# Kernel optimization log

Measured on AMD Instinct MI355X. Metric: run time of the kernel, lower is better.

Reference implementation:

```python
import jax, jax.numpy as jnp
import numpy as np

N_EMBD = 128
N_HEAD = 4
HEAD_DIM = N_EMBD // N_HEAD  # 32


def setup_inputs() -> dict:
    key = jax.random.key(0)
    k_x, k_wqkv, k_bqkv, k_wp, k_bp = jax.random.split(key, 5)
    B, T = 8, 2048
    x = jax.random.normal(k_x, (B, T, N_EMBD), dtype=jnp.float32)
    # torch Linear(n_embd, 3*n_embd): weight [out,in]; store as [in,out] for x @ W
    scale = 1.0 / np.sqrt(N_EMBD)
    w_qkv = jax.random.uniform(k_wqkv, (N_EMBD, 3 * N_EMBD), minval=-scale, maxval=scale, dtype=jnp.float32)
    b_qkv = jax.random.uniform(k_bqkv, (3 * N_EMBD,), minval=-scale, maxval=scale, dtype=jnp.float32)
    w_proj = jax.random.uniform(k_wp, (N_EMBD, N_EMBD), minval=-scale, maxval=scale, dtype=jnp.float32)
    b_proj = jax.random.uniform(k_bp, (N_EMBD,), minval=-scale, maxval=scale, dtype=jnp.float32)
    return {"x": x, "w_qkv": w_qkv, "b_qkv": b_qkv, "w_proj": w_proj, "b_proj": b_proj}


def reference(x, w_qkv, b_qkv, w_proj, b_proj):
    B, T, C = x.shape
    H, D = N_HEAD, HEAD_DIM
    qkv = x @ w_qkv + b_qkv  # [B,T,3C]
    q, k, v = jnp.split(qkv, 3, axis=2)
    # [B,T,C] -> [B,H,T,D]
    q = q.reshape(B, T, H, D).transpose(0, 2, 1, 3)
    k = k.reshape(B, T, H, D).transpose(0, 2, 1, 3)
    v = v.reshape(B, T, H, D).transpose(0, 2, 1, 3)
    scale = 1.0 / np.sqrt(D).astype(np.float32)
    logits = jnp.einsum("bhqd,bhkd->bhqk", q, k) * scale  # [B,H,T,T]
    causal = jnp.tril(jnp.ones((T, T), dtype=bool))
    logits = jnp.where(causal, logits, jnp.finfo(logits.dtype).min)
    attn = jax.nn.softmax(logits, axis=-1)
    y = jnp.einsum("bhqk,bhkd->bhqd", attn, v)  # [B,H,T,D]
    y = y.transpose(0, 2, 1, 3).reshape(B, T, C)
    y = y @ w_proj + b_proj
    # dropout is identity in eval/inference mode
    return y
```

## Files before the change

### kernel.cpp

```cpp
#include <hip/hip_runtime.h>
#include <hip/hip_bf16.h>
#include <stdint.h>


#define T_SEQ 2048
#define C_EMBD 128
#define NH 4
#define HD 32
#define BATCH 8
#define BHT (BATCH * NH)

typedef float f4  __attribute__((ext_vector_type(4)));
typedef short bh8 __attribute__((ext_vector_type(8)));
typedef unsigned long long ull;

__device__ __forceinline__ unsigned short f2bf(float f) {
    union { float f; unsigned u; } v; v.f = f;
    return (unsigned short)((v.u + 0x7fffu + ((v.u >> 16) & 1u)) >> 16);
}
__device__ __forceinline__ ull pk4(float a, float b, float c, float d) {
    return (ull)f2bf(a) | ((ull)f2bf(b) << 16) | ((ull)f2bf(c) << 32) | ((ull)f2bf(d) << 48);
}

__global__ __launch_bounds__(256) void qkv_mfma(const float* __restrict__ x,
                                                const float* __restrict__ w,
                                                const float* __restrict__ bias,
                                                unsigned short* __restrict__ qb,
                                                unsigned short* __restrict__ kb,
                                                unsigned short* __restrict__ vtb) {
    constexpr int XR = 136;
    constexpr int WR = 136;
    constexpr int VR = 72;
    __shared__ __align__(16) unsigned short xs[64 * XR];
    __shared__ __align__(16) unsigned short wt[128 * WR];
    __shared__ __align__(16) unsigned short vt[128 * VR];

    const int nt = blockIdx.x;
    const int mt = blockIdx.y;
    const int t0g = mt * 64;
    const int b = t0g >> 11;
    const int t0 = t0g & 2047;
    const int tid = threadIdx.x;
    const int wave = tid >> 6;
    const int lane = tid & 63;
    const int col = lane & 15;
    const int quad = lane >> 4;

    for (int i = 0; i < 8; ++i) {
        const int idx = tid + i * 256;
        const int row = idx >> 5, c4 = idx & 31;
        const float4 xv = *(const float4*)(x + (size_t)(t0g + row) * C_EMBD + c4 * 4);
        *(ull*)(&xs[row * XR + c4 * 4]) = pk4(xv.x, xv.y, xv.z, xv.w);
    }
    for (int i = 0; i < 16; ++i) {
        const int idx = tid + i * 256;
        const int n = idx & 127, k4 = idx >> 7;
        const float w0 = w[(k4 * 4 + 0) * 384 + nt * 128 + n];
        const float w1 = w[(k4 * 4 + 1) * 384 + nt * 128 + n];
        const float w2 = w[(k4 * 4 + 2) * 384 + nt * 128 + n];
        const float w3 = w[(k4 * 4 + 3) * 384 + nt * 128 + n];
        *(ull*)(&wt[n * WR + k4 * 4]) = pk4(w0, w1, w2, w3);
    }
    __syncthreads();

    f4 acc[8];
#pragma unroll
    for (int nf = 0; nf < 8; ++nf) {
        const float bv = bias[nt * 128 + nf * 16 + col];
        acc[nf] = (f4){bv, bv, bv, bv};
    }
#pragma unroll
    for (int ch = 0; ch < 4; ++ch) {
        const bh8 af = *(const bh8*)(&xs[(wave * 16 + col) * XR + ch * 32 + quad * 8]);
#pragma unroll
        for (int nf = 0; nf < 8; ++nf) {
            const bh8 bf = *(const bh8*)(&wt[(nf * 16 + col) * WR + ch * 32 + quad * 8]);
            acc[nf] = __builtin_amdgcn_mfma_f32_16x16x32_bf16(af, bf, acc[nf], 0, 0, 0);
        }
    }

    const int mrow = wave * 16 + quad * 4;
    if (nt < 2) {
        unsigned short* outp = (nt == 0) ? qb : kb;
        const float sc = (nt == 0) ? 0.25503485952317864f : 1.0f;
#pragma unroll
        for (int nf = 0; nf < 8; ++nf) {
            const int n = nf * 16 + col, h = n >> 5, d = n & 31;
            const size_t base = ((size_t)(b * NH + h) * T_SEQ + t0 + mrow) * HD + d;
#pragma unroll
            for (int r = 0; r < 4; ++r)
                outp[base + (size_t)r * HD] = f2bf(acc[nf][r] * sc);
        }
    } else {
#pragma unroll
        for (int nf = 0; nf < 8; ++nf) {
            const int n = nf * 16 + col;
#pragma unroll
            for (int r = 0; r < 4; ++r)
                vt[n * VR + mrow + r] = f2bf(acc[nf][r]);
        }
        __syncthreads();
        for (int i = 0; i < 16; ++i) {
            const int idx = tid + i * 256;
            const int c = idx >> 5, dw = idx & 31;
            const int h2 = c >> 5, d2 = c & 31;
            const unsigned v0 = *(const unsigned*)(&vt[c * VR + dw * 2]);
            *(unsigned*)(vtb + ((size_t)(b * NH + h2) * HD + d2) * T_SEQ + t0 + dw * 2) = v0;
        }
    }
}

__global__ __launch_bounds__(256, 4) void attn(const unsigned short* __restrict__ qb,
                                               const unsigned short* __restrict__ kb,
                                               const unsigned short* __restrict__ vtb,
                                               unsigned short* __restrict__ y) {
    constexpr int KROW = 40;
    constexpr int VROW = 72;
    constexpr int PROW = 72;
    __shared__ __align__(16) unsigned short Ks[2][64 * KROW];
    __shared__ __align__(16) unsigned short Vt[2][32 * VROW];
    __shared__ __align__(16) unsigned short Pb[4][16 * PROW];

    const int bid = blockIdx.x;
    const int bh = bid & 31;
    const int pr = bid >> 5;
    const int tid = threadIdx.x;
    const int wave = tid >> 6;
    const int lane = tid & 63;
    const int col = lane & 15;
    const int quad = lane >> 4;

    const unsigned short* kbase = kb + (size_t)bh * T_SEQ * HD;
    const unsigned short* vbase = vtb + (size_t)bh * HD * T_SEQ;
    const int ks_t = tid >> 2, ks_q = tid & 3;
    const int vs_d = tid >> 3, vs_s = tid & 7;

    for (int ph = 0; ph < 2; ++ph) {
        const int qt = ph ? pr : (31 - pr);
        const int q0 = qt * 64;
        const int ntiles = qt + 1;

        const bh8 qfrag = *(const bh8*)(qb + ((size_t)bh * T_SEQ + q0 + wave * 16 + col) * HD + quad * 8);
        f4 yacc0 = {0.f, 0.f, 0.f, 0.f}, yacc1 = {0.f, 0.f, 0.f, 0.f};
        float rs[4] = {0.f, 0.f, 0.f, 0.f};

        uint4 kreg = *(const uint4*)(kbase + (size_t)ks_t * HD + ks_q * 8);
        uint4 vreg = *(const uint4*)(vbase + (size_t)vs_d * T_SEQ + vs_s * 8);

        for (int kt = 0; kt < ntiles; ++kt) {
            const int buf = kt & 1;
            *(uint4*)(&Ks[buf][ks_t * KROW + ks_q * 8]) = kreg;
            *(uint4*)(&Vt[buf][vs_d * VROW + vs_s * 8]) = vreg;
            if (kt + 1 < ntiles) {
                kreg = *(const uint4*)(kbase + (size_t)((kt + 1) * 64 + ks_t) * HD + ks_q * 8);
                vreg = *(const uint4*)(vbase + (size_t)vs_d * T_SEQ + (kt + 1) * 64 + vs_s * 8);
            }
            __syncthreads();

            const bool diag = (kt == qt);
            f4 z[4];
#pragma unroll
            for (int f = 0; f < 4; ++f) {
                if (diag && f > wave) {
                    z[f] = (f4){-1e30f, -1e30f, -1e30f, -1e30f};
                } else {
                    const bh8 kfrag = *(const bh8*)(&Ks[buf][(f * 16 + col) * KROW + quad * 8]);
                    f4 zz = {0.f, 0.f, 0.f, 0.f};
                    zz = __builtin_amdgcn_mfma_f32_16x16x32_bf16(qfrag, kfrag, zz, 0, 0, 0);
                    if (diag && f == wave) {
#pragma unroll
                        for (int r = 0; r < 4; ++r)
                            if (col > quad * 4 + r) zz[r] = -1e30f;
                    }
                    z[f] = zz;
                }
            }
#pragma unroll
            for (int f = 0; f < 4; ++f)
#pragma unroll
                for (int r = 0; r < 4; ++r) {
                    const float pv = __builtin_amdgcn_exp2f(z[f][r]);
                    rs[r] += pv;
                    Pb[wave][(quad * 4 + r) * PROW + f * 16 + col] = f2bf(pv);
                }
#pragma unroll
            for (int kk = 0; kk < 2; ++kk) {
                const bh8 pf = *(const bh8*)(&Pb[wave][col * PROW + kk * 32 + quad * 8]);
                const bh8 v0 = *(const bh8*)(&Vt[buf][col * VROW + kk * 32 + quad * 8]);
                yacc0 = __builtin_amdgcn_mfma_f32_16x16x32_bf16(pf, v0, yacc0, 0, 0, 0);
                const bh8 v1 = *(const bh8*)(&Vt[buf][(16 + col) * VROW + kk * 32 + quad * 8]);
                yacc1 = __builtin_amdgcn_mfma_f32_16x16x32_bf16(pf, v1, yacc1, 0, 0, 0);
            }
        }

        const int bb = bh >> 2, hh = bh & 3;
        unsigned short* yp = y + ((size_t)bb * T_SEQ + q0 + wave * 16) * C_EMBD + hh * HD;
#pragma unroll
        for (int r = 0; r < 4; ++r) {
            float t = rs[r];
            t += __shfl_xor(t, 1);
            t += __shfl_xor(t, 2);
            t += __shfl_xor(t, 4);
            t += __shfl_xor(t, 8);
            const float inv = 1.0f / t;
            yp[(quad * 4 + r) * C_EMBD + col] = f2bf(yacc0[r] * inv);
            yp[(quad * 4 + r) * C_EMBD + 16 + col] = f2bf(yacc1[r] * inv);
        }
        __syncthreads();
    }
}

__global__ __launch_bounds__(256) void out_mfma(const unsigned short* __restrict__ y,
                                                const float* __restrict__ w,
                                                const float* __restrict__ bias,
                                                float* __restrict__ out) {
    constexpr int YR = 136;
    constexpr int WR = 136;
    __shared__ __align__(16) unsigned short ys[64 * YR];
    __shared__ __align__(16) unsigned short wt[128 * WR];

    const int mt = blockIdx.x;
    const int row0 = mt * 64;
    const int tid = threadIdx.x;
    const int wave = tid >> 6;
    const int lane = tid & 63;
    const int col = lane & 15;
    const int quad = lane >> 4;

    for (int i = 0; i < 4; ++i) {
        const int idx = tid + i * 256;
        const int row = idx >> 4, q8 = idx & 15;
        const uint4 v = *(const uint4*)(y + (size_t)(row0 + row) * C_EMBD + q8 * 8);
        *(uint4*)(&ys[row * YR + q8 * 8]) = v;
    }
    for (int i = 0; i < 16; ++i) {
        const int idx = tid + i * 256;
        const int n = idx & 127, k4 = idx >> 7;
        const float w0 = w[(k4 * 4 + 0) * C_EMBD + n];
        const float w1 = w[(k4 * 4 + 1) * C_EMBD + n];
        const float w2 = w[(k4 * 4 + 2) * C_EMBD + n];
        const float w3 = w[(k4 * 4 + 3) * C_EMBD + n];
        *(ull*)(&wt[n * WR + k4 * 4]) = pk4(w0, w1, w2, w3);
    }
    __syncthreads();

    f4 acc[8];
#pragma unroll
    for (int nf = 0; nf < 8; ++nf) {
        const float bv = bias[nf * 16 + col];
        acc[nf] = (f4){bv, bv, bv, bv};
    }
#pragma unroll
    for (int ch = 0; ch < 4; ++ch) {
        const bh8 af = *(const bh8*)(&ys[(wave * 16 + col) * YR + ch * 32 + quad * 8]);
#pragma unroll
        for (int nf = 0; nf < 8; ++nf) {
            const bh8 bf = *(const bh8*)(&wt[(nf * 16 + col) * WR + ch * 32 + quad * 8]);
            acc[nf] = __builtin_amdgcn_mfma_f32_16x16x32_bf16(af, bf, acc[nf], 0, 0, 0);
        }
    }

    const int mrow = wave * 16 + quad * 4;
#pragma unroll
    for (int nf = 0; nf < 8; ++nf)
#pragma unroll
        for (int r = 0; r < 4; ++r)
            out[(size_t)(row0 + mrow + r) * C_EMBD + nf * 16 + col] = acc[nf][r];
}

extern "C" void kernel_launch(void* const* d_in, const int* in_sizes, int n_in,
                              void* d_out, int out_size, void* d_ws, size_t ws_size,
                              hipStream_t stream) {
    const float* x      = (const float*)d_in[0];
    const float* w_qkv  = (const float*)d_in[1];
    const float* b_qkv  = (const float*)d_in[2];
    const float* w_proj = (const float*)d_in[3];
    const float* b_proj = (const float*)d_in[4];
    float* out = (float*)d_out;

    unsigned short* qb  = (unsigned short*)d_ws;
    unsigned short* kb  = qb + (size_t)BHT * T_SEQ * HD;
    unsigned short* vtb = kb + (size_t)BHT * T_SEQ * HD;
    unsigned short* yb  = vtb + (size_t)BHT * T_SEQ * HD;

    qkv_mfma<<<dim3(3, 256), 256, 0, stream>>>(x, w_qkv, b_qkv, qb, kb, vtb);
    attn<<<512, 256, 0, stream>>>(qb, kb, vtb, yb);
    out_mfma<<<256, 256, 0, stream>>>(yb, w_proj, b_proj, out);
}
```

Before: 110.9 us.

## Compute transposed QK^T, pack P with cvt_pk_bf16, one query tile per block

The attention kernel swaps the QK^T MFMA operands, so each lane holds four consecutive keys for a single query. This lets the row sum be a scalar and the P tile be written with one 64-bit store of hardware-packed bf16 pairs instead of 16 scalar stores. The two-tile load-balancing loop per block is removed, and the grid is doubled to one query tile per block. That adds parallelism but loses the pairing of long and short causal tiles, so scheduling of the uneven work is left to the hardware.

```diff
diff --git a/kernel.cpp b/kernel.cpp
--- a/kernel.cpp
+++ b/kernel.cpp
@@ -20,6 +20,11 @@
 }
 __device__ __forceinline__ ull pk4(float a, float b, float c, float d) {
     return (ull)f2bf(a) | ((ull)f2bf(b) << 16) | ((ull)f2bf(c) << 32) | ((ull)f2bf(d) << 48);
+}
+__device__ __forceinline__ unsigned cvt_pk_bf16(float a, float b) {
+    unsigned r;
+    asm("v_cvt_pk_bf16_f32 %0, %1, %2" : "=v"(r) : "v"(a), "v"(b));
+    return r;
 }
 
 __global__ __launch_bounds__(256) void qkv_mfma(const float* __restrict__ x,
@@ -123,7 +128,7 @@
 
     const int bid = blockIdx.x;
     const int bh = bid & 31;
-    const int pr = bid >> 5;
+    const int qt = 31 - (bid >> 5);
     const int tid = threadIdx.x;
     const int wave = tid >> 6;
     const int lane = tid & 63;
@@ -135,78 +140,76 @@
     const int ks_t = tid >> 2, ks_q = tid & 3;
     const int vs_d = tid >> 3, vs_s = tid & 7;
 
-    for (int ph = 0; ph < 2; ++ph) {
-        const int qt = ph ? pr : (31 - pr);
-        const int q0 = qt * 64;
-        const int ntiles = qt + 1;
-
-        const bh8 qfrag = *(const bh8*)(qb + ((size_t)bh * T_SEQ + q0 + wave * 16 + col) * HD + quad * 8);
-        f4 yacc0 = {0.f, 0.f, 0.f, 0.f}, yacc1 = {0.f, 0.f, 0.f, 0.f};
-        float rs[4] = {0.f, 0.f, 0.f, 0.f};
-
-        uint4 kreg = *(const uint4*)(kbase + (size_t)ks_t * HD + ks_q * 8);
-        uint4 vreg = *(const uint4*)(vbase + (size_t)vs_d * T_SEQ + vs_s * 8);
-
-        for (int kt = 0; kt < ntiles; ++kt) {
-            const int buf = kt & 1;
-            *(uint4*)(&Ks[buf][ks_t * KROW + ks_q * 8]) = kreg;
-            *(uint4*)(&Vt[buf][vs_d * VROW + vs_s * 8]) = vreg;
-            if (kt + 1 < ntiles) {
-                kreg = *(const uint4*)(kbase + (size_t)((kt + 1) * 64 + ks_t) * HD + ks_q * 8);
-                vreg = *(const uint4*)(vbase + (size_t)vs_d * T_SEQ + (kt + 1) * 64 + vs_s * 8);
+    const int q0 = qt * 64;
+    const int ntiles = qt + 1;
+
+    const bh8 qfrag = *(const bh8*)(qb + ((size_t)bh * T_SEQ + q0 + wave * 16 + col) * HD + quad * 8);
+    f4 yacc0 = {0.f, 0.f, 0.f, 0.f}, yacc1 = {0.f, 0.f, 0.f, 0.f};
+    float rs = 0.f;
+
+    uint4 kreg = *(const uint4*)(kbase + (size_t)ks_t * HD + ks_q * 8);
+    uint4 vreg = *(const uint4*)(vbase + (size_t)vs_d * T_SEQ + vs_s * 8);
+
+    for (int kt = 0; kt < ntiles; ++kt) {
+        const int buf = kt & 1;
+        *(uint4*)(&Ks[buf][ks_t * KROW + ks_q * 8]) = kreg;
+        *(uint4*)(&Vt[buf][vs_d * VROW + vs_s * 8]) = vreg;
+        if (kt + 1 < ntiles) {
+            kreg = *(const uint4*)(kbase + (size_t)((kt + 1) * 64 + ks_t) * HD + ks_q * 8);
+            vreg = *(const uint4*)(vbase + (size_t)vs_d * T_SEQ + (kt + 1) * 64 + vs_s * 8);
+        }
+        __syncthreads();
+
+        const bool diag = (kt == qt);
+        f4 z[4];
+#pragma unroll
+        for (int f = 0; f < 4; ++f) {
+            if (diag && f > wave) {
+                z[f] = (f4){-1e30f, -1e30f, -1e30f, -1e30f};
+            } else {
+                const bh8 kfrag = *(const bh8*)(&Ks[buf][(f * 16 + col) * KROW + quad * 8]);
+                f4 zz = {0.f, 0.f, 0.f, 0.f};
+                zz = __builtin_amdgcn_mfma_f32_16x16x32_bf16(kfrag, qfrag, zz, 0, 0, 0);
+                if (diag && f == wave) {
+#pragma unroll
+                    for (int r = 0; r < 4; ++r)
+                        if (quad * 4 + r > col) zz[r] = -1e30f;
+                }
+                z[f] = zz;
             }
-            __syncthreads();
-
-            const bool diag = (kt == qt);
-            f4 z[4];
-#pragma unroll
-            for (int f = 0; f < 4; ++f) {
-                if (diag && f > wave) {
-                    z[f] = (f4){-1e30f, -1e30f, -1e30f, -1e30f};
-                } else {
-                    const bh8 kfrag = *(const bh8*)(&Ks[buf][(f * 16 + col) * KROW + quad * 8]);
-                    f4 zz = {0.f, 0.f, 0.f, 0.f};
-                    zz = __builtin_amdgcn_mfma_f32_16x16x32_bf16(qfrag, kfrag, zz, 0, 0, 0);
-                    if (diag && f == wave) {
-#pragma unroll
-                        for (int r = 0; r < 4; ++r)
-                            if (col > quad * 4 + r) zz[r] = -1e30f;
-                    }
-                    z[f] = zz;
-                }
-            }
-#pragma unroll
-            for (int f = 0; f < 4; ++f)
-#pragma unroll
-                for (int r = 0; r < 4; ++r) {
-                    const float pv = __builtin_amdgcn_exp2f(z[f][r]);
-                    rs[r] += pv;
-                    Pb[wave][(quad * 4 + r) * PROW + f * 16 + col] = f2bf(pv);
-                }
-#pragma unroll
-            for (int kk = 0; kk < 2; ++kk) {
-                const bh8 pf = *(const bh8*)(&Pb[wave][col * PROW + kk * 32 + quad * 8]);
-                const bh8 v0 = *(const bh8*)(&Vt[buf][col * VROW + kk * 32 + quad * 8]);
-                yacc0 = __builtin_amdgcn_mfma_f32_16x16x32_bf16(pf, v0, yacc0, 0, 0, 0);
-                const bh8 v1 = *(const bh8*)(&Vt[buf][(16 + col) * VROW + kk * 32 + quad * 8]);
-                yacc1 = __builtin_amdgcn_mfma_f32_16x16x32_bf16(pf, v1, yacc1, 0, 0, 0);
-            }
-        }
-
-        const int bb = bh >> 2, hh = bh & 3;
-        unsigned short* yp = y + ((size_t)bb * T_SEQ + q0 + wave * 16) * C_EMBD + hh * HD;
-#pragma unroll
-        for (int r = 0; r < 4; ++r) {
-            float t = rs[r];
-            t += __shfl_xor(t, 1);
-            t += __shfl_xor(t, 2);
-            t += __shfl_xor(t, 4);
-            t += __shfl_xor(t, 8);
-            const float inv = 1.0f / t;
-            yp[(quad * 4 + r) * C_EMBD + col] = f2bf(yacc0[r] * inv);
-            yp[(quad * 4 + r) * C_EMBD + 16 + col] = f2bf(yacc1[r] * inv);
-        }
-        __syncthreads();
+        }
+#pragma unroll
+        for (int f = 0; f < 4; ++f) {
+            const float p0 = __builtin_amdgcn_exp2f(z[f][0]);
+            const float p1 = __builtin_amdgcn_exp2f(z[f][1]);
+            const float p2 = __builtin_amdgcn_exp2f(z[f][2]);
+            const float p3 = __builtin_amdgcn_exp2f(z[f][3]);
+            rs += (p0 + p1) + (p2 + p3);
+            const unsigned d01 = cvt_pk_bf16(p0, p1);
+            const unsigned d23 = cvt_pk_bf16(p2, p3);
+            *(ull*)(&Pb[wave][col * PROW + f * 16 + quad * 4]) = (ull)d01 | ((ull)d23 << 32);
+        }
+#pragma unroll
+        for (int kk = 0; kk < 2; ++kk) {
+            const bh8 pf = *(const bh8*)(&Pb[wave][col * PROW + kk * 32 + quad * 8]);
+            const bh8 v0 = *(const bh8*)(&Vt[buf][col * VROW + kk * 32 + quad * 8]);
+            yacc0 = __builtin_amdgcn_mfma_f32_16x16x32_bf16(pf, v0, yacc0, 0, 0, 0);
+            const bh8 v1 = *(const bh8*)(&Vt[buf][(16 + col) * VROW + kk * 32 + quad * 8]);
+            yacc1 = __builtin_amdgcn_mfma_f32_16x16x32_bf16(pf, v1, yacc1, 0, 0, 0);
+        }
+    }
+
+    rs += __shfl_xor(rs, 16);
+    rs += __shfl_xor(rs, 32);
+    const float inv = 1.0f / rs;
+
+    const int bb = bh >> 2, hh = bh & 3;
+    unsigned short* yp = y + ((size_t)bb * T_SEQ + q0 + wave * 16) * C_EMBD + hh * HD;
+#pragma unroll
+    for (int r = 0; r < 4; ++r) {
+        const float invr = __shfl(inv, (lane & 48) | (quad * 4 + r));
+        yp[(quad * 4 + r) * C_EMBD + col] = f2bf(yacc0[r] * invr);
+        yp[(quad * 4 + r) * C_EMBD + 16 + col] = f2bf(yacc1[r] * invr);
     }
 }
 
@@ -284,6 +287,6 @@
     unsigned short* yb  = vtb + (size_t)BHT * T_SEQ * HD;
 
     qkv_mfma<<<dim3(3, 256), 256, 0, stream>>>(x, w_qkv, b_qkv, qb, kb, vtb);
-    attn<<<512, 256, 0, stream>>>(qb, kb, vtb, yb);
+    attn<<<1024, 256, 0, stream>>>(qb, kb, vtb, yb);
     out_mfma<<<256, 256, 0, stream>>>(yb, w_proj, b_proj, out);
 }
```

Result: faster. 106.3 us (-4.2%).
